# Optimization experiments

Measured on AMD Instinct MI355X. Metric: run time of the kernel, lower is better.

The kernel has to match this reference:

```python
import jax, jax.numpy as jnp
import numpy as np

D_MODEL = 1024
NHEAD = 16
HEAD_DIM = D_MODEL // NHEAD


def setup_inputs() -> dict:
    key = jax.random.key(0)
    ks = jax.random.split(key, 11)
    B, S = 4, 2048
    s = 1.0 / np.sqrt(D_MODEL)
    return {
        "q": jax.random.normal(ks[0], (B, S, D_MODEL), jnp.float32),
        "k": jax.random.normal(ks[1], (B, S, D_MODEL), jnp.float32),
        "v": jax.random.normal(ks[2], (B, S, D_MODEL), jnp.float32),
        "Wq": jax.random.normal(ks[3], (D_MODEL, D_MODEL), jnp.float32) * s,
        "bq": jnp.zeros((D_MODEL,), jnp.float32),
        "Wk": jax.random.normal(ks[4], (D_MODEL, D_MODEL), jnp.float32) * s,
        "bk": jnp.zeros((D_MODEL,), jnp.float32),
        "Wv": jax.random.normal(ks[5], (D_MODEL, D_MODEL), jnp.float32) * s,
        "bv": jnp.zeros((D_MODEL,), jnp.float32),
        "Wo": jax.random.normal(ks[6], (D_MODEL, D_MODEL), jnp.float32) * s,
        "bo": jnp.zeros((D_MODEL,), jnp.float32),
    }


def reference(q, k, v, Wq, bq, Wk, bk, Wv, bv, Wo, bo):
    B, S, _ = q.shape
    H, Dh = NHEAD, HEAD_DIM

    def proj(x, W, b):  # nn.Linear: x @ W.T + b, then split heads -> [B,H,S,Dh]
        y = x @ W.T + b
        return y.reshape(B, S, H, Dh).transpose(0, 2, 1, 3)

    qh = proj(q, Wq, bq)
    kh = proj(k, Wk, bk)
    vh = proj(v, Wv, bv)

    scores = jnp.einsum("bhsd,bhtd->bhst", qh, kh) / jnp.sqrt(jnp.float32(Dh))
    attn = jax.nn.softmax(scores, axis=-1)
    out = jnp.einsum("bhst,bhtd->bhsd", attn, vh)  # [B,H,S,Dh]
    out = out.transpose(0, 2, 1, 3).reshape(B, S, H * Dh)
    return out @ Wo.T + bo
```

## Files before the change

### kernel.cpp

```cpp
#include <hip/hip_runtime.h>


typedef short bf16x8 __attribute__((ext_vector_type(8)));
typedef short bf16x4 __attribute__((ext_vector_type(4)));
typedef float f32x4 __attribute__((ext_vector_type(4)));
typedef float f32x16 __attribute__((ext_vector_type(16)));
typedef unsigned int u32x4 __attribute__((ext_vector_type(4)));

__device__ __forceinline__ short f2bf(float x) {
    union { float f; unsigned int u; } un; un.f = x;
    unsigned int u = un.u;
    return (short)(unsigned short)((u + 0x7fffu + ((u >> 16) & 1u)) >> 16);
}

__device__ __forceinline__ void gll16(const void* g, void* l) {
    __builtin_amdgcn_global_load_lds(
        (const __attribute__((address_space(1))) void*)g,
        (__attribute__((address_space(3))) void*)l, 16, 0, 0);
}

__device__ __forceinline__ void plswap(unsigned& a, unsigned& b) {
    asm("v_permlane32_swap_b32 %0, %1" : "+v"(a), "+v"(b));
}

#define SBAR()   asm volatile("s_barrier" ::: "memory")
#define VMCNT6() asm volatile("s_waitcnt vmcnt(6)" ::: "memory")

struct CvtArgs { const float* s[4]; unsigned short* d[4]; int n4; };
__global__ __launch_bounds__(256) void cvt_bf16(CvtArgs ca) {
    const float* s = ca.s[blockIdx.y];
    unsigned short* d = ca.d[blockIdx.y];
    int i = blockIdx.x * blockDim.x + threadIdx.x;
    int stride = gridDim.x * blockDim.x;
    const float4* s4 = reinterpret_cast<const float4*>(s);
    bf16x4* d4 = reinterpret_cast<bf16x4*>(d);
    for (; i < ca.n4; i += stride) {
        float4 x = s4[i];
        bf16x4 y;
        y[0] = f2bf(x.x); y[1] = f2bf(x.y); y[2] = f2bf(x.z); y[3] = f2bf(x.w);
        d4[i] = y;
    }
}

__device__ __forceinline__ void gemm_core(const unsigned short* __restrict__ A,
                                          const unsigned short* __restrict__ W,
                                          const float* __restrict__ bias,
                                          float scale, void* __restrict__ out,
                                          int mode) {
    __shared__ unsigned short As[3 * 128 * 64];
    __shared__ unsigned short Bs[3 * 256 * 64];
    const int tid = threadIdx.x;
    const int orid = blockIdx.x + 4 * blockIdx.y;
    const int swz = ((orid & 7) << 5) | (orid >> 3);
    const int n0 = (swz & 3) * 256;
    const int m0 = (swz >> 2) * 128;
    const int wave = tid >> 6, lane = tid & 63;
    const int wmr = (wave >> 2) * 64, wnr = (wave & 3) * 64;
    const int l15 = lane & 15, quad = lane >> 4;
    const int cb = l15 & 7;
    const int srow = tid >> 3;
    const int scol = ((tid & 7) ^ (srow & 7)) * 8;

    f32x4 acc[4][4] = {};

#define SA(kt, sl)                                                                  \
    {                                                                               \
        gll16(&A[(size_t)(m0 + srow) * 1024 + (kt) * 64 + scol],                    \
              &As[(sl) * 8192 + tid * 8]);                                          \
        gll16(&A[(size_t)(m0 + 64 + srow) * 1024 + (kt) * 64 + scol],               \
              &As[(sl) * 8192 + 4096 + tid * 8]);                                   \
    }
#define SB(kt, sl, ro)                                                              \
    gll16(&W[(size_t)(n0 + (ro) * 64 + srow) * 1024 + (kt) * 64 + scol],            \
          &Bs[(sl) * 16384 + (ro) * 4096 + tid * 8]);

    SA(0, 0); SB(0, 0, 0); SB(0, 0, 1); SB(0, 0, 2); SB(0, 0, 3);
    SA(1, 1); SB(1, 1, 0); SB(1, 1, 1); SB(1, 1, 2); SB(1, 1, 3);
    VMCNT6();
    __builtin_amdgcn_sched_barrier(0);
    SBAR();
    __builtin_amdgcn_sched_barrier(0);

    int sl = 0;
    for (int kt = 0; kt < 16; ++kt) {
        const int ss = (sl + 2 >= 3) ? sl - 1 : sl + 2;
        const unsigned short* Ab = &As[sl * 8192];
        const unsigned short* Bb = &Bs[sl * 16384];
        {
            const int co = (quad ^ cb) * 8;
            bf16x8 a[4], b[4];
#pragma unroll
            for (int i = 0; i < 4; ++i)
                a[i] = *reinterpret_cast<const bf16x8*>(&Ab[(wmr + i * 16 + l15) * 64 + co]);
#pragma unroll
            for (int j = 0; j < 4; ++j)
                b[j] = *reinterpret_cast<const bf16x8*>(&Bb[(wnr + j * 16 + l15) * 64 + co]);
            if (kt < 14) { SA(kt + 2, ss); SB(kt + 2, ss, 0); }
            SBAR();
            __builtin_amdgcn_sched_barrier(0);
            __builtin_amdgcn_s_setprio(1);
#pragma unroll
            for (int i = 0; i < 4; ++i)
#pragma unroll
                for (int j = 0; j < 4; ++j)
                    acc[i][j] = __builtin_amdgcn_mfma_f32_16x16x32_bf16(a[i], b[j], acc[i][j], 0, 0, 0);
            __builtin_amdgcn_s_setprio(0);
            SBAR();
            __builtin_amdgcn_sched_barrier(0);
        }
        {
            const int co = ((4 + quad) ^ cb) * 8;
            bf16x8 a[4], b[4];
#pragma unroll
            for (int i = 0; i < 4; ++i)
                a[i] = *reinterpret_cast<const bf16x8*>(&Ab[(wmr + i * 16 + l15) * 64 + co]);
#pragma unroll
            for (int j = 0; j < 4; ++j)
                b[j] = *reinterpret_cast<const bf16x8*>(&Bb[(wnr + j * 16 + l15) * 64 + co]);
            if (kt < 14) { SB(kt + 2, ss, 1); SB(kt + 2, ss, 2); SB(kt + 2, ss, 3); }
            if (kt < 15) {
                VMCNT6();
                __builtin_amdgcn_sched_barrier(0);
            }
            SBAR();
            __builtin_amdgcn_sched_barrier(0);
            __builtin_amdgcn_s_setprio(1);
#pragma unroll
            for (int i = 0; i < 4; ++i)
#pragma unroll
                for (int j = 0; j < 4; ++j)
                    acc[i][j] = __builtin_amdgcn_mfma_f32_16x16x32_bf16(a[i], b[j], acc[i][j], 0, 0, 0);
            __builtin_amdgcn_s_setprio(0);
            SBAR();
            __builtin_amdgcn_sched_barrier(0);
        }
        sl = (sl + 1 == 3) ? 0 : sl + 1;
    }
#undef SA
#undef SB

#pragma unroll
    for (int i = 0; i < 4; ++i) {
#pragma unroll
        for (int j = 0; j < 4; ++j) {
#pragma unroll
            for (int r = 0; r < 4; ++r) {
                int m = m0 + wmr + i * 16 + quad * 4 + r;
                int n = n0 + wnr + j * 16 + l15;
                float val = (acc[i][j][r] + bias[n]) * scale;
                if (mode == 0) {
                    reinterpret_cast<float*>(out)[(size_t)m * 1024 + n] = val;
                } else {
                    int b_ = m >> 11, s = m & 2047, h = n >> 6, d = n & 63;
                    size_t off = (mode == 1)
                                     ? ((size_t)((b_ * 16 + h) * 2048 + s) * 64 + d)
                                     : ((size_t)((b_ * 16 + h) * 64 + d) * 2048 + s);
                    reinterpret_cast<unsigned short*>(out)[off] = (unsigned short)f2bf(val);
                }
            }
        }
    }
}

struct QkvArgs {
    const unsigned short* A[3];
    const unsigned short* W[3];
    const float* bias[3];
    float scale[3];
    unsigned short* out[3];
    int mode[3];
};
__global__ __launch_bounds__(512, 2) void gemm_qkv(QkvArgs ga) {
    int z = blockIdx.z;
    gemm_core(ga.A[z], ga.W[z], ga.bias[z], ga.scale[z], ga.out[z], ga.mode[z]);
}

__global__ __launch_bounds__(512, 2) void gemm_wo(const unsigned short* __restrict__ A,
                                                  const unsigned short* __restrict__ W,
                                                  const float* __restrict__ bias,
                                                  float* __restrict__ out) {
    gemm_core(A, W, bias, 1.0f, out, 0);
}


#define SOFTMAX_PV(MT, VBASE)                                                        \
    {                                                                                \
        float e[16];                                                                 \
        _Pragma("unroll")                                                            \
        for (int r = 0; r < 16; ++r) e[r] = __builtin_amdgcn_exp2f(sacc[MT][r]);     \
        lacc += ((e[0] + e[1]) + (e[2] + e[3])) + ((e[4] + e[5]) + (e[6] + e[7])) +  \
                ((e[8] + e[9]) + (e[10] + e[11])) + ((e[12] + e[13]) + (e[14] + e[15])); \
        unsigned w[8];                                                               \
        _Pragma("unroll")                                                            \
        for (int t = 0; t < 8; ++t) {                                                \
            union { float f; unsigned u; } a0{e[2 * t]}, a1{e[2 * t + 1]};           \
            w[t] = __builtin_amdgcn_perm(a1.u + 0x8000u, a0.u + 0x8000u, 0x07060302u); \
        }                                                                            \
        plswap(w[0], w[2]); plswap(w[1], w[3]);                                      \
        plswap(w[4], w[6]); plswap(w[5], w[7]);                                      \
        u32x4 t0; t0[0] = w[0]; t0[1] = w[1]; t0[2] = w[2]; t0[3] = w[3];            \
        u32x4 t1; t1[0] = w[4]; t1[1] = w[5]; t1[2] = w[6]; t1[3] = w[7];            \
        bf16x8 pa0 = __builtin_bit_cast(bf16x8, t0);                                 \
        bf16x8 pa1 = __builtin_bit_cast(bf16x8, t1);                                 \
        __builtin_amdgcn_s_setprio(1);                                               \
        _Pragma("unroll")                                                            \
        for (int nt = 0; nt < 2; ++nt) {                                             \
            bf16x8 bv0 = *reinterpret_cast<const bf16x8*>(&(VBASE)[rowoff[nt] + chx[2 * (MT)]]); \
            bf16x8 bv1 = *reinterpret_cast<const bf16x8*>(&(VBASE)[rowoff[nt] + chx[2 * (MT) + 1]]); \
            o[nt] = __builtin_amdgcn_mfma_f32_32x32x16_bf16(pa0, bv0, o[nt], 0, 0, 0); \
            o[nt] = __builtin_amdgcn_mfma_f32_32x32x16_bf16(pa1, bv1, o[nt], 0, 0, 0); \
        }                                                                            \
        __builtin_amdgcn_s_setprio(0);                                               \
    }

#define QK_TILE(KBASE)                                                               \
    {                                                                                \
        f32x16 zz = {};                                                              \
        sacc[0] = zz; sacc[1] = zz;                                                  \
        __builtin_amdgcn_s_setprio(1);                                               \
        _Pragma("unroll")                                                            \
        for (int c = 0; c < 4; ++c) {                                                \
            bf16x8 ak0 = *reinterpret_cast<const bf16x8*>(&(KBASE)[rowoff[0] + chx[c]]); \
            bf16x8 ak1 = *reinterpret_cast<const bf16x8*>(&(KBASE)[rowoff[1] + chx[c]]); \
            sacc[0] = __builtin_amdgcn_mfma_f32_32x32x16_bf16(ak0, qreg[c], sacc[0], 0, 0, 0); \
            sacc[1] = __builtin_amdgcn_mfma_f32_32x32x16_bf16(ak1, qreg[c], sacc[1], 0, 0, 0); \
        }                                                                            \
        __builtin_amdgcn_s_setprio(0);                                               \
    }

__global__ __launch_bounds__(256, 4) void flash_attn(const unsigned short* __restrict__ Qh,
                                                     const unsigned short* __restrict__ Kh,
                                                     const unsigned short* __restrict__ Vt,
                                                     unsigned short* __restrict__ Oa) {
    __shared__ unsigned short Ks[2][64 * 64];
    __shared__ unsigned short Vs[2][64 * 64];
    const int tid = threadIdx.x;
    const int bh = blockIdx.y;
    const int q0 = blockIdx.x * 128;
    const unsigned short* Qb = Qh + (size_t)bh * 2048 * 64;
    const unsigned short* Kb = Kh + (size_t)bh * 2048 * 64;
    const unsigned short* Vb = Vt + (size_t)bh * 64 * 2048;
    const int wave = tid >> 6, lane = tid & 63;
    const int l31 = lane & 31, hi = lane >> 5;
    const int wq = wave * 32;
    const int srow = tid >> 3;
    const int scol = ((tid & 7) ^ (srow & 7)) * 8;

    int chx[4], rowoff[2];
#pragma unroll
    for (int c = 0; c < 4; ++c) chx[c] = ((c * 2 + hi) ^ (l31 & 7)) * 8;
    rowoff[0] = l31 * 64;
    rowoff[1] = (32 + l31) * 64;

    bf16x8 qreg[4];
#pragma unroll
    for (int c = 0; c < 4; ++c)
        qreg[c] = *reinterpret_cast<const bf16x8*>(
            &Qb[(size_t)(q0 + wq + l31) * 64 + c * 16 + hi * 8]);

    f32x16 o[2] = {};
    f32x16 sacc[2];
    float lacc = 0.f;

#pragma unroll
    for (int ro = 0; ro < 2; ++ro) {
        gll16(&Kb[(size_t)(ro * 32 + srow) * 64 + scol], &Ks[0][ro * 2048 + tid * 8]);
        gll16(&Vb[(size_t)(ro * 32 + srow) * 2048 + scol], &Vs[0][ro * 2048 + tid * 8]);
        gll16(&Kb[(size_t)(64 + ro * 32 + srow) * 64 + scol], &Ks[1][ro * 2048 + tid * 8]);
    }
    __syncthreads();
    QK_TILE(Ks[0]);
    __syncthreads();

    for (int it = 0; it < 31; ++it) {
        const int cur = it & 1, nxt = cur ^ 1;
        if (it < 30) {
            const int kvn = (it + 2) * 64;
#pragma unroll
            for (int ro = 0; ro < 2; ++ro)
                gll16(&Kb[(size_t)(kvn + ro * 32 + srow) * 64 + scol], &Ks[cur][ro * 2048 + tid * 8]);
        }
        {
            const int kvn = (it + 1) * 64;
#pragma unroll
            for (int ro = 0; ro < 2; ++ro)
                gll16(&Vb[(size_t)(ro * 32 + srow) * 2048 + kvn + scol], &Vs[nxt][ro * 2048 + tid * 8]);
        }

        SOFTMAX_PV(0, Vs[cur]);
        SOFTMAX_PV(1, Vs[cur]);

        QK_TILE(Ks[nxt]);

        __syncthreads();
    }
    SOFTMAX_PV(0, Vs[1]);
    SOFTMAX_PV(1, Vs[1]);

    float lfull = lacc + __shfl_xor(lacc, 32, 64);
    float rinv = 1.0f / lfull;
    const int b_ = bh >> 4, h = bh & 15;
#pragma unroll
    for (int r = 0; r < 16; ++r) {
        const int qrow = (r & 3) + 8 * (r >> 2) + 4 * hi;
        const float rl = __shfl(rinv, qrow, 64);
        const int s = q0 + wq + qrow;
#pragma unroll
        for (int nt = 0; nt < 2; ++nt) {
            const int d = nt * 32 + l31;
            Oa[(size_t)(b_ * 2048 + s) * 1024 + h * 64 + d] =
                (unsigned short)f2bf(o[nt][r] * rl);
        }
    }
}

extern "C" void kernel_launch(void* const* d_in, const int* in_sizes, int n_in,
                              void* d_out, int out_size, void* d_ws, size_t ws_size,
                              hipStream_t stream) {
    const float* q  = (const float*)d_in[0];
    const float* k  = (const float*)d_in[1];
    const float* v  = (const float*)d_in[2];
    const float* Wq = (const float*)d_in[3];
    const float* bq = (const float*)d_in[4];
    const float* Wk = (const float*)d_in[5];
    const float* bk = (const float*)d_in[6];
    const float* Wv = (const float*)d_in[7];
    const float* bv = (const float*)d_in[8];
    const float* Wo = (const float*)d_in[9];
    const float* bo = (const float*)d_in[10];

    const size_t E = (size_t)8192 * 1024;
    const size_t WE = (size_t)1024 * 1024;
    unsigned short* r0 = (unsigned short*)d_ws;
    unsigned short* r1 = r0 + E;
    unsigned short* r2 = r1 + E;
    unsigned short* r3 = r2 + E;
    unsigned short* wqb = r3 + E;
    unsigned short* wkb = wqb + WE;
    unsigned short* wvb = wkb + WE;
    unsigned short* wob = wvb + WE;

    CvtArgs ca;
    ca.s[0] = q; ca.d[0] = r0;
    ca.s[1] = k; ca.d[1] = r1;
    ca.s[2] = v; ca.d[2] = r2;
    ca.s[3] = q; ca.d[3] = r0;
    ca.n4 = (int)(E / 4);
    cvt_bf16<<<dim3(1024, 3), 256, 0, stream>>>(ca);

    CvtArgs cw;
    cw.s[0] = Wq; cw.d[0] = wqb;
    cw.s[1] = Wk; cw.d[1] = wkb;
    cw.s[2] = Wv; cw.d[2] = wvb;
    cw.s[3] = Wo; cw.d[3] = wob;
    cw.n4 = (int)(WE / 4);
    cvt_bf16<<<dim3(256, 4), 256, 0, stream>>>(cw);

    const float QSCALE = 0.125f * 1.44269504088896340736f;

    QkvArgs ga;
    ga.A[0] = r0; ga.W[0] = wqb; ga.bias[0] = bq; ga.scale[0] = QSCALE; ga.out[0] = r3; ga.mode[0] = 1;
    ga.A[1] = r1; ga.W[1] = wkb; ga.bias[1] = bk; ga.scale[1] = 1.0f;   ga.out[1] = r0; ga.mode[1] = 1;
    ga.A[2] = r2; ga.W[2] = wvb; ga.bias[2] = bv; ga.scale[2] = 1.0f;   ga.out[2] = r1; ga.mode[2] = 2;
    gemm_qkv<<<dim3(4, 64, 3), 512, 0, stream>>>(ga);

    flash_attn<<<dim3(16, 64), 256, 0, stream>>>(r3, r0, r1, r2);
    gemm_wo<<<dim3(4, 64), 512, 0, stream>>>(r2, wob, bo, (float*)d_out);
}
```

Baseline: 349.7 us.

## Use smaller 128x128 double-buffered GEMM tiles for the QKV projection

Adds a second GEMM core with 128x128 output tiles, 256 threads, a two-stage LDS double buffer and a simpler prefetch loop, and uses it for the fused QKV projection launch (grid 8x64x3). The output-projection GEMM keeps the original 128x256 triple-buffered core. The goal is more blocks and better occupancy and load balance on the QKV GEMM, at the cost of less data reuse per tile and a shallower prefetch pipeline.

```diff
diff --git a/kernel.cpp b/kernel.cpp
--- a/kernel.cpp
+++ b/kernel.cpp
@@ -42,11 +42,91 @@
     }
 }
 
-__device__ __forceinline__ void gemm_core(const unsigned short* __restrict__ A,
-                                          const unsigned short* __restrict__ W,
-                                          const float* __restrict__ bias,
-                                          float scale, void* __restrict__ out,
-                                          int mode) {
+__device__ __forceinline__ void gemm_core2(const unsigned short* __restrict__ A,
+                                           const unsigned short* __restrict__ W,
+                                           const float* __restrict__ bias,
+                                           float scale, void* __restrict__ out,
+                                           int mode) {
+    __shared__ unsigned short As[2][128 * 64];
+    __shared__ unsigned short Bs[2][128 * 64];
+    const int tid = threadIdx.x;
+    const int orid = blockIdx.x + 8 * blockIdx.y;
+    const int swz = ((orid & 7) << 6) | (orid >> 3);
+    const int n0 = (swz & 7) * 128;
+    const int m0 = (swz >> 3) * 128;
+    const int wave = tid >> 6, lane = tid & 63;
+    const int wm = (wave >> 1) * 64, wn = (wave & 1) * 64;
+    const int l15 = lane & 15, quad = lane >> 4;
+    const int srow = tid >> 3;
+    const int scol = ((tid & 7) ^ (srow & 7)) * 8;
+    const int cb = l15 & 7;
+
+    f32x4 acc[4][4] = {};
+
+#pragma unroll
+    for (int ro = 0; ro < 4; ++ro) {
+        gll16(&A[(size_t)(m0 + ro * 32 + srow) * 1024 + scol], &As[0][ro * 2048 + tid * 8]);
+        gll16(&W[(size_t)(n0 + ro * 32 + srow) * 1024 + scol], &Bs[0][ro * 2048 + tid * 8]);
+    }
+    __syncthreads();
+
+    for (int kt = 0; kt < 16; ++kt) {
+        const int cur = kt & 1;
+        if (kt < 15) {
+            const int k0 = (kt + 1) * 64;
+#pragma unroll
+            for (int ro = 0; ro < 4; ++ro) {
+                gll16(&A[(size_t)(m0 + ro * 32 + srow) * 1024 + k0 + scol], &As[cur ^ 1][ro * 2048 + tid * 8]);
+                gll16(&W[(size_t)(n0 + ro * 32 + srow) * 1024 + k0 + scol], &Bs[cur ^ 1][ro * 2048 + tid * 8]);
+            }
+        }
+#pragma unroll
+        for (int kk = 0; kk < 2; ++kk) {
+            const int co = ((4 * kk + quad) ^ cb) * 8;
+            bf16x8 a[4], b[4];
+#pragma unroll
+            for (int i = 0; i < 4; ++i)
+                a[i] = *reinterpret_cast<bf16x8*>(&As[cur][(wm + i * 16 + l15) * 64 + co]);
+#pragma unroll
+            for (int j = 0; j < 4; ++j)
+                b[j] = *reinterpret_cast<bf16x8*>(&Bs[cur][(wn + j * 16 + l15) * 64 + co]);
+#pragma unroll
+            for (int i = 0; i < 4; ++i)
+#pragma unroll
+                for (int j = 0; j < 4; ++j)
+                    acc[i][j] = __builtin_amdgcn_mfma_f32_16x16x32_bf16(a[i], b[j], acc[i][j], 0, 0, 0);
+        }
+        __syncthreads();
+    }
+
+#pragma unroll
+    for (int i = 0; i < 4; ++i) {
+#pragma unroll
+        for (int j = 0; j < 4; ++j) {
+#pragma unroll
+            for (int r = 0; r < 4; ++r) {
+                int m = m0 + wm + i * 16 + quad * 4 + r;
+                int n = n0 + wn + j * 16 + l15;
+                float val = (acc[i][j][r] + bias[n]) * scale;
+                if (mode == 0) {
+                    reinterpret_cast<float*>(out)[(size_t)m * 1024 + n] = val;
+                } else {
+                    int b_ = m >> 11, s = m & 2047, h = n >> 6, d = n & 63;
+                    size_t off = (mode == 1)
+                                     ? ((size_t)((b_ * 16 + h) * 2048 + s) * 64 + d)
+                                     : ((size_t)((b_ * 16 + h) * 64 + d) * 2048 + s);
+                    reinterpret_cast<unsigned short*>(out)[off] = (unsigned short)f2bf(val);
+                }
+            }
+        }
+    }
+}
+
+__device__ __forceinline__ void gemm_core8(const unsigned short* __restrict__ A,
+                                           const unsigned short* __restrict__ W,
+                                           const float* __restrict__ bias,
+                                           float scale, void* __restrict__ out,
+                                           int mode) {
     __shared__ unsigned short As[3 * 128 * 64];
     __shared__ unsigned short Bs[3 * 256 * 64];
     const int tid = threadIdx.x;
@@ -170,16 +250,16 @@
     unsigned short* out[3];
     int mode[3];
 };
-__global__ __launch_bounds__(512, 2) void gemm_qkv(QkvArgs ga) {
+__global__ __launch_bounds__(256) void gemm_qkv(QkvArgs ga) {
     int z = blockIdx.z;
-    gemm_core(ga.A[z], ga.W[z], ga.bias[z], ga.scale[z], ga.out[z], ga.mode[z]);
+    gemm_core2(ga.A[z], ga.W[z], ga.bias[z], ga.scale[z], ga.out[z], ga.mode[z]);
 }
 
 __global__ __launch_bounds__(512, 2) void gemm_wo(const unsigned short* __restrict__ A,
                                                   const unsigned short* __restrict__ W,
                                                   const float* __restrict__ bias,
                                                   float* __restrict__ out) {
-    gemm_core(A, W, bias, 1.0f, out, 0);
+    gemm_core8(A, W, bias, 1.0f, out, 0);
 }
 
 
@@ -362,7 +442,7 @@
     ga.A[0] = r0; ga.W[0] = wqb; ga.bias[0] = bq; ga.scale[0] = QSCALE; ga.out[0] = r3; ga.mode[0] = 1;
     ga.A[1] = r1; ga.W[1] = wkb; ga.bias[1] = bk; ga.scale[1] = 1.0f;   ga.out[1] = r0; ga.mode[1] = 1;
     ga.A[2] = r2; ga.W[2] = wvb; ga.bias[2] = bv; ga.scale[2] = 1.0f;   ga.out[2] = r1; ga.mode[2] = 2;
-    gemm_qkv<<<dim3(4, 64, 3), 512, 0, stream>>>(ga);
+    gemm_qkv<<<dim3(8, 64, 3), 256, 0, stream>>>(ga);
 
     flash_attn<<<dim3(16, 64), 256, 0, stream>>>(r3, r0, r1, r2);
     gemm_wo<<<dim3(4, 64), 512, 0, stream>>>(r2, wob, bo, (float*)d_out);
```

After: 357.3 us. +2.2%, slower.
